# Kernel tuning notes

Hardware: AMD Instinct MI355X
Metric: run time of the kernel (lower is better)

The kernel has to match this reference:

```python
import jax, jax.numpy as jnp
import numpy as np

GROUP = 128  # int4 quant group size and Hadamard block size

# Sylvester Hadamard matrix of size 128, orthonormal (H @ H.T = I)
_h = np.array([[1.0]], dtype=np.float32)
while _h.shape[0] < GROUP:
    _h = np.kron(_h, np.array([[1.0, 1.0], [1.0, -1.0]], dtype=np.float32))
H128 = jnp.asarray(_h / np.sqrt(GROUP))


def hadamard_rotate(x):
    # blockwise Hadamard rotation along the last dim (last dim % 128 == 0)
    *lead, n = x.shape
    xr = x.reshape(*lead, n // GROUP, GROUP) @ H128
    return xr.reshape(*lead, n)


def dequant_int4(wq, scales):
    # wq: [out, in] uint4 values in [0,16); scales: [out, in//GROUP]
    out_dim, in_dim = wq.shape
    w = (wq.astype(jnp.float32) - 8.0).reshape(out_dim, in_dim // GROUP, GROUP)
    w = w * scales[:, :, None]
    return w.reshape(out_dim, in_dim)


def rotate_linear_int4(x, wq, scales):
    # y = hadamard(x) @ dequant(W).T
    return hadamard_rotate(x) @ dequant_int4(wq, scales).T


def setup_inputs() -> dict:
    key = jax.random.key(0)
    ks = jax.random.split(key, 7)
    T, D, I = 4096, 4096, 12288  # tokens, hidden, intermediate
    x = jax.random.normal(ks[0], (T, D), dtype=jnp.float32)
    wq_gate = jax.random.randint(ks[1], (I, D), 0, 16, dtype=jnp.int32)
    s_gate = jax.random.uniform(ks[2], (I, D // GROUP), dtype=jnp.float32) * 0.01
    wq_up = jax.random.randint(ks[3], (I, D), 0, 16, dtype=jnp.int32)
    s_up = jax.random.uniform(ks[4], (I, D // GROUP), dtype=jnp.float32) * 0.01
    wq_down = jax.random.randint(ks[5], (D, I), 0, 16, dtype=jnp.int32)
    s_down = jax.random.uniform(ks[6], (D, I // GROUP), dtype=jnp.float32) * 0.01
    return {"x": x, "wq_gate": wq_gate, "s_gate": s_gate,
            "wq_up": wq_up, "s_up": s_up,
            "wq_down": wq_down, "s_down": s_down}


def reference(x, wq_gate, s_gate, wq_up, s_up, wq_down, s_down):
    gate = rotate_linear_int4(x, wq_gate, s_gate)   # [T, I]
    up = rotate_linear_int4(x, wq_up, s_up)         # [T, I]
    h = jax.nn.silu(gate) * up                       # SiluAndMul on cat([gate, up])
    return rotate_linear_int4(h, wq_down, s_down)    # [T, D]
```

## Files before the change

kernel.cpp:

```cpp
#include <hip/hip_runtime.h>
#include <hip/hip_bf16.h>
#include <cstdint>

#define T_DIM 4096
#define D_DIM 4096
#define I_DIM 12288
#define GRP   128

typedef __attribute__((ext_vector_type(8))) short bf16x8;
typedef __attribute__((ext_vector_type(4))) float f32x4;
typedef __attribute__((ext_vector_type(4))) int   int32x4;

typedef __attribute__((address_space(3))) void lds_void;
typedef const __attribute__((address_space(1))) void gmem_void;

static __device__ __forceinline__ unsigned short f2bf(float f) {
    unsigned int u = __float_as_uint(f);
    u += 0x7FFFu + ((u >> 16) & 1u);
    return (unsigned short)(u >> 16);
}
static __device__ __forceinline__ float bf2f(unsigned short b) {
    return __uint_as_float(((unsigned int)b) << 16);
}

__global__ void had_f32_to_bf16(const float* __restrict__ in, unsigned short* __restrict__ out,
                                int ngroups) {
    int gid = blockIdx.x * (blockDim.x >> 6) + (threadIdx.x >> 6);
    if (gid >= ngroups) return;
    int lane = threadIdx.x & 63;
    const float2 v2 = *reinterpret_cast<const float2*>(in + (size_t)gid * 128 + lane * 2);
    float v0 = v2.x, v1 = v2.y;
    { float t0 = v0 + v1, t1 = v0 - v1; v0 = t0; v1 = t1; }
#pragma unroll
    for (int m = 1; m <= 32; m <<= 1) {
        float b0 = __shfl_xor(v0, m);
        float b1 = __shfl_xor(v1, m);
        if (lane & m) { v0 = b0 - v0; v1 = b1 - v1; }
        else          { v0 = v0 + b0; v1 = v1 + b1; }
    }
    const float s = 0.08838834764831843f;
    unsigned int o = (unsigned int)f2bf(v0 * s) | ((unsigned int)f2bf(v1 * s) << 16);
    *reinterpret_cast<unsigned int*>(out + (size_t)gid * 128 + lane * 2) = o;
}

__global__ void had_bf16_inplace(unsigned short* __restrict__ buf, int ngroups) {
    int gid = blockIdx.x * (blockDim.x >> 6) + (threadIdx.x >> 6);
    if (gid >= ngroups) return;
    int lane = threadIdx.x & 63;
    unsigned int pv = *reinterpret_cast<const unsigned int*>(buf + (size_t)gid * 128 + lane * 2);
    float v0 = __uint_as_float((pv & 0xFFFFu) << 16);
    float v1 = __uint_as_float(pv & 0xFFFF0000u);
    { float t0 = v0 + v1, t1 = v0 - v1; v0 = t0; v1 = t1; }
#pragma unroll
    for (int m = 1; m <= 32; m <<= 1) {
        float b0 = __shfl_xor(v0, m);
        float b1 = __shfl_xor(v1, m);
        if (lane & m) { v0 = b0 - v0; v1 = b1 - v1; }
        else          { v0 = v0 + b0; v1 = v1 + b1; }
    }
    const float s = 0.08838834764831843f;
    unsigned int o = (unsigned int)f2bf(v0 * s) | ((unsigned int)f2bf(v1 * s) << 16);
    *reinterpret_cast<unsigned int*>(buf + (size_t)gid * 128 + lane * 2) = o;
}

__global__ void dequant_w(const int* __restrict__ Wq, const float* __restrict__ S,
                          unsigned short* __restrict__ Wbf, int In, int total8) {
    int t = blockIdx.x * blockDim.x + threadIdx.x;
    if (t >= total8) return;
    size_t base = (size_t)t * 8;
    size_t row = base / (size_t)In;
    int col = (int)(base - row * (size_t)In);
    float sc = S[row * (size_t)(In >> 7) + (col >> 7)];
    const int32x4* p = reinterpret_cast<const int32x4*>(Wq + base);
    int32x4 a = p[0], b = p[1];
    float nsc = -8.0f * sc;
    unsigned int o0 = (unsigned int)f2bf((float)a.x * sc + nsc) |
                      ((unsigned int)f2bf((float)a.y * sc + nsc) << 16);
    unsigned int o1 = (unsigned int)f2bf((float)a.z * sc + nsc) |
                      ((unsigned int)f2bf((float)a.w * sc + nsc) << 16);
    unsigned int o2 = (unsigned int)f2bf((float)b.x * sc + nsc) |
                      ((unsigned int)f2bf((float)b.y * sc + nsc) << 16);
    unsigned int o3 = (unsigned int)f2bf((float)b.z * sc + nsc) |
                      ((unsigned int)f2bf((float)b.w * sc + nsc) << 16);
    *reinterpret_cast<uint4*>(Wbf + base) = make_uint4(o0, o1, o2, o3);
}


#define GBAR()  __builtin_amdgcn_s_barrier()
#define VMW(n)  asm volatile("s_waitcnt vmcnt(" #n ")" ::: "memory")
#define P1()    __builtin_amdgcn_s_setprio(1)
#define P0()    __builtin_amdgcn_s_setprio(0)

#define STG(bb, mat, h, kb)                                                            \
  { _Pragma("unroll")                                                                  \
    for (int i_ = 0; i_ < 2; ++i_) {                                                   \
      const int rl_ = (h) * 128 + i_ * 64 + (tid >> 3);                                \
      const int gs_ = (tid & 7) ^ ((tid >> 3) & 7);                                    \
      const unsigned short* gp_ = ((mat) ? W : A) +                                    \
          (size_t)(((mat) ? n0 : m0) + rl_) * K + (kb) + gs_ * 8;                      \
      unsigned short* lp_ = lds + (bb) * 32768 + (mat) * 16384 +                       \
          ((h) * 128 + i_ * 64 + wid * 8) * 64;                                        \
      __builtin_amdgcn_global_load_lds((gmem_void*)gp_, (lds_void*)lp_, 16, 0, 0);     \
    } }

#define LDAQ(dst, bb, q)                                                               \
  _Pragma("unroll")                                                                    \
  for (int mi_ = 0; mi_ < 2; ++mi_)                                                    \
  _Pragma("unroll")                                                                    \
  for (int ks_ = 0; ks_ < 2; ++ks_) {                                                  \
    int r_ = wr * 128 + (q) * 32 + mi_ * 16 + (lane & 15);                             \
    int c_ = ks_ * 4 + kc;                                                             \
    dst[mi_][ks_] = *reinterpret_cast<const bf16x8*>(                                  \
        lds + (bb) * 32768 + r_ * 64 + ((c_ ^ (r_ & 7)) << 3));                        \
  }

#define LDBQ(bb)                                                                       \
  _Pragma("unroll")                                                                    \
  for (int ni_ = 0; ni_ < 4; ++ni_)                                                    \
  _Pragma("unroll")                                                                    \
  for (int ks_ = 0; ks_ < 2; ++ks_) {                                                  \
    int r_ = wc * 64 + ni_ * 16 + (lane & 15);                                         \
    int c_ = ks_ * 4 + kc;                                                             \
    bk[ni_][ks_] = *reinterpret_cast<const bf16x8*>(                                   \
        lds + (bb) * 32768 + 16384 + r_ * 64 + ((c_ ^ (r_ & 7)) << 3));                \
  }

#define MF16(q, afb)                                                                   \
  _Pragma("unroll")                                                                    \
  for (int ks_ = 0; ks_ < 2; ++ks_)                                                    \
  _Pragma("unroll")                                                                    \
  for (int mi_ = 0; mi_ < 2; ++mi_)                                                    \
  _Pragma("unroll")                                                                    \
  for (int ni_ = 0; ni_ < 4; ++ni_)                                                    \
    acc[(q) * 2 + mi_][ni_] = __builtin_amdgcn_mfma_f32_16x16x32_bf16(                 \
        afb[mi_][ks_], bk[ni_][ks_], acc[(q) * 2 + mi_][ni_], 0, 0, 0);

template<int MODE>
__global__ __launch_bounds__(512, 2)
void gemm256(const unsigned short* __restrict__ A,
             const unsigned short* __restrict__ W,
             void* __restrict__ C, int M, int N, int K)
{
    __shared__ __align__(16) unsigned short lds[65536];

    const int MT = M >> 8;
    const int nwg = gridDim.x;
    const int bid = blockIdx.x;
    const int cpx = nwg >> 3;
    const int wg  = (bid & 7) * cpx + (bid >> 3);
    const int m0 = (wg % MT) << 8;
    const int n0 = (wg / MT) << 8;

    const int tid  = threadIdx.x;
    const int lane = tid & 63;
    const int wid  = tid >> 6;
    const int wr = wid >> 2;
    const int wc = wid & 3;
    const int kc = lane >> 4;

    f32x4 acc[8][4];
#pragma unroll
    for (int i = 0; i < 8; ++i)
#pragma unroll
        for (int j = 0; j < 4; ++j) acc[i][j] = (f32x4)0.0f;

    const int NT = K >> 6;
    const int J  = NT >> 1;

    bf16x8 afA[2][2], afB[2][2], bk[4][2];

    STG(0, 0, 0, 0); STG(0, 0, 1, 0);
    STG(0, 1, 0, 0); STG(0, 1, 1, 0);
    VMW(0);
    GBAR();
    LDAQ(afA, 0, 0);
    STG(1, 1, 0, 64); STG(1, 1, 1, 64);

    for (int j = 0; j < J - 1; ++j) {
        const int ka  = (j << 7);
        const int kb1 = ka + 64;
        const int ka2 = ka + 128;
        const int ka3 = ka + 192;
        LDBQ(0); LDAQ(afB, 0, 1); STG(1, 0, 0, kb1);
        GBAR(); P1(); MF16(0, afA); P0(); GBAR();
        LDAQ(afA, 0, 2); STG(1, 0, 1, kb1);
        GBAR(); P1(); MF16(1, afB); P0(); GBAR();
        LDAQ(afB, 0, 3); STG(0, 1, 0, ka2);
        GBAR(); P1(); MF16(2, afA); P0(); GBAR();
        VMW(2); LDAQ(afA, 1, 0); STG(0, 1, 1, ka2);
        GBAR(); P1(); MF16(3, afB); P0(); GBAR();
        LDBQ(1); LDAQ(afB, 1, 1); STG(0, 0, 0, ka2);
        GBAR(); P1(); MF16(0, afA); P0(); GBAR();
        LDAQ(afA, 1, 2); STG(0, 0, 1, ka2);
        GBAR(); P1(); MF16(1, afB); P0(); GBAR();
        LDAQ(afB, 1, 3); STG(1, 1, 0, ka3);
        GBAR(); P1(); MF16(2, afA); P0(); GBAR();
        VMW(2); LDAQ(afA, 0, 0); STG(1, 1, 1, ka3);
        GBAR(); P1(); MF16(3, afB); P0(); GBAR();
    }

    {
        const int kb1 = ((NT - 1) << 6);
        LDBQ(0); LDAQ(afB, 0, 1); STG(1, 0, 0, kb1);
        GBAR(); P1(); MF16(0, afA); P0(); GBAR();
        LDAQ(afA, 0, 2); STG(1, 0, 1, kb1);
        GBAR(); P1(); MF16(1, afB); P0(); GBAR();
        LDAQ(afB, 0, 3);
        GBAR(); P1(); MF16(2, afA); P0(); GBAR();
        VMW(0); LDAQ(afA, 1, 0);
        GBAR(); P1(); MF16(3, afB); P0(); GBAR();
        LDBQ(1); LDAQ(afB, 1, 1);
        GBAR(); P1(); MF16(0, afA); P0(); GBAR();
        LDAQ(afA, 1, 2);
        GBAR(); P1(); MF16(1, afB); P0(); GBAR();
        LDAQ(afB, 1, 3);
        GBAR(); P1(); MF16(2, afA); P0(); GBAR();
        GBAR(); P1(); MF16(3, afB); P0();
    }

#pragma unroll
    for (int mi = 0; mi < 8; ++mi)
#pragma unroll
        for (int ni = 0; ni < 4; ++ni) {
            const int col = n0 + (wc << 6) + ni * 16 + (lane & 15);
#pragma unroll
            for (int r = 0; r < 4; ++r) {
                const int row = m0 + (wr << 7) + mi * 16 + ((lane >> 4) << 2) + r;
                const size_t idx = (size_t)row * N + col;
                if (MODE == 2) {
                    ((float*)C)[idx] = acc[mi][ni][r];
                } else if (MODE == 0) {
                    ((unsigned short*)C)[idx] = f2bf(acc[mi][ni][r]);
                } else {
                    float g = bf2f(((unsigned short*)C)[idx]);
                    float u = acc[mi][ni][r];
                    float h = (g / (1.0f + __expf(-g))) * u;
                    ((unsigned short*)C)[idx] = f2bf(h);
                }
            }
        }
}

__global__ __launch_bounds__(256, 2)
void gemm_gateup_fb(const unsigned short* __restrict__ Xr,
                    const int* __restrict__ Wg, const float* __restrict__ Sg,
                    const int* __restrict__ Wu, const float* __restrict__ Su,
                    unsigned short* __restrict__ H)
{
    __shared__ __align__(16) unsigned short lA [128 * 64];
    __shared__ __align__(16) unsigned short lBg[128 * 64];
    __shared__ __align__(16) unsigned short lBu[128 * 64];
    const int MT = T_DIM / 128;
    const int bid = blockIdx.x;
    const int m0 = (bid % MT) * 128;
    const int n0 = (bid / MT) * 128;
    const int tid  = threadIdx.x;
    const int lane = tid & 63;
    const int wid  = tid >> 6;
    const int wr = wid >> 1, wc = wid & 1;
    f32x4 accG[4][4], accU[4][4];
#pragma unroll
    for (int i = 0; i < 4; ++i)
#pragma unroll
        for (int j = 0; j < 4; ++j) { accG[i][j] = (f32x4)0.0f; accU[i][j] = (f32x4)0.0f; }
    const int arow = lane >> 3;
    const int acol = (lane & 7) * 8;
    const int SStride = D_DIM / GRP;
    for (int k0 = 0; k0 < D_DIM; k0 += 64) {
        __syncthreads();
#pragma unroll
        for (int it = 0; it < 4; ++it) {
            int chunk = wid * 4 + it;
            const unsigned short* gp = Xr + (size_t)(m0 + chunk * 8 + arow) * D_DIM + k0 + acol;
            __builtin_amdgcn_global_load_lds((gmem_void*)gp, (lds_void*)(lA + chunk * 512), 16, 0, 0);
        }
        const int g = k0 >> 7;
#pragma unroll
        for (int i = 0; i < 8; ++i) {
            int linear = i * 1024 + tid * 4;
            int r = linear >> 6;
            int c = linear & 63;
            const int32x4 wg = *reinterpret_cast<const int32x4*>(Wg + (size_t)(n0 + r) * D_DIM + k0 + c);
            const int32x4 wu = *reinterpret_cast<const int32x4*>(Wu + (size_t)(n0 + r) * D_DIM + k0 + c);
            float scg = Sg[(size_t)(n0 + r) * SStride + g];
            float scu = Su[(size_t)(n0 + r) * SStride + g];
            unsigned int g01 = (unsigned int)f2bf((float)(wg.x - 8) * scg) | ((unsigned int)f2bf((float)(wg.y - 8) * scg) << 16);
            unsigned int g23 = (unsigned int)f2bf((float)(wg.z - 8) * scg) | ((unsigned int)f2bf((float)(wg.w - 8) * scg) << 16);
            unsigned int u01 = (unsigned int)f2bf((float)(wu.x - 8) * scu) | ((unsigned int)f2bf((float)(wu.y - 8) * scu) << 16);
            unsigned int u23 = (unsigned int)f2bf((float)(wu.z - 8) * scu) | ((unsigned int)f2bf((float)(wu.w - 8) * scu) << 16);
            *reinterpret_cast<uint2*>(lBg + r * 64 + c) = make_uint2(g01, g23);
            *reinterpret_cast<uint2*>(lBu + r * 64 + c) = make_uint2(u01, u23);
        }
        __syncthreads();
#pragma unroll
        for (int ks = 0; ks < 2; ++ks) {
            const int koff = ks * 32 + (lane >> 4) * 8;
            bf16x8 af[4], bg[4], bu[4];
#pragma unroll
            for (int mi = 0; mi < 4; ++mi)
                af[mi] = *reinterpret_cast<const bf16x8*>(lA + (wr * 64 + mi * 16 + (lane & 15)) * 64 + koff);
#pragma unroll
            for (int ni = 0; ni < 4; ++ni) {
                bg[ni] = *reinterpret_cast<const bf16x8*>(lBg + (wc * 64 + ni * 16 + (lane & 15)) * 64 + koff);
                bu[ni] = *reinterpret_cast<const bf16x8*>(lBu + (wc * 64 + ni * 16 + (lane & 15)) * 64 + koff);
            }
#pragma unroll
            for (int mi = 0; mi < 4; ++mi)
#pragma unroll
                for (int ni = 0; ni < 4; ++ni) {
                    accG[mi][ni] = __builtin_amdgcn_mfma_f32_16x16x32_bf16(af[mi], bg[ni], accG[mi][ni], 0, 0, 0);
                    accU[mi][ni] = __builtin_amdgcn_mfma_f32_16x16x32_bf16(af[mi], bu[ni], accU[mi][ni], 0, 0, 0);
                }
        }
    }
#pragma unroll
    for (int mi = 0; mi < 4; ++mi)
#pragma unroll
        for (int ni = 0; ni < 4; ++ni) {
            const int col = n0 + wc * 64 + ni * 16 + (lane & 15);
#pragma unroll
            for (int r = 0; r < 4; ++r) {
                const int row = m0 + wr * 64 + mi * 16 + (lane >> 4) * 4 + r;
                float gv = accG[mi][ni][r];
                float uv = accU[mi][ni][r];
                float hv = (gv / (1.0f + __expf(-gv))) * uv;
                H[(size_t)row * I_DIM + col] = f2bf(hv);
            }
        }
}

__global__ __launch_bounds__(256, 2)
void gemm_down_fb(const unsigned short* __restrict__ Hr,
                  const int* __restrict__ Wd, const float* __restrict__ Sd,
                  float* __restrict__ Out)
{
    __shared__ __align__(16) unsigned short lA[128 * 64];
    __shared__ __align__(16) unsigned short lB[128 * 64];
    const int MT = T_DIM / 128;
    const int bid = blockIdx.x;
    const int m0 = (bid % MT) * 128;
    const int n0 = (bid / MT) * 128;
    const int tid  = threadIdx.x;
    const int lane = tid & 63;
    const int wid  = tid >> 6;
    const int wr = wid >> 1, wc = wid & 1;
    f32x4 acc[4][4];
#pragma unroll
    for (int i = 0; i < 4; ++i)
#pragma unroll
        for (int j = 0; j < 4; ++j) acc[i][j] = (f32x4)0.0f;
    const int arow = lane >> 3;
    const int acol = (lane & 7) * 8;
    const int SStride = I_DIM / GRP;
    for (int k0 = 0; k0 < I_DIM; k0 += 64) {
        __syncthreads();
#pragma unroll
        for (int it = 0; it < 4; ++it) {
            int chunk = wid * 4 + it;
            const unsigned short* gp = Hr + (size_t)(m0 + chunk * 8 + arow) * I_DIM + k0 + acol;
            __builtin_amdgcn_global_load_lds((gmem_void*)gp, (lds_void*)(lA + chunk * 512), 16, 0, 0);
        }
        const int g = k0 >> 7;
#pragma unroll
        for (int i = 0; i < 8; ++i) {
            int linear = i * 1024 + tid * 4;
            int r = linear >> 6;
            int c = linear & 63;
            const int32x4 wd = *reinterpret_cast<const int32x4*>(Wd + (size_t)(n0 + r) * I_DIM + k0 + c);
            float sc = Sd[(size_t)(n0 + r) * SStride + g];
            unsigned int d01 = (unsigned int)f2bf((float)(wd.x - 8) * sc) | ((unsigned int)f2bf((float)(wd.y - 8) * sc) << 16);
            unsigned int d23 = (unsigned int)f2bf((float)(wd.z - 8) * sc) | ((unsigned int)f2bf((float)(wd.w - 8) * sc) << 16);
            *reinterpret_cast<uint2*>(lB + r * 64 + c) = make_uint2(d01, d23);
        }
        __syncthreads();
#pragma unroll
        for (int ks = 0; ks < 2; ++ks) {
            const int koff = ks * 32 + (lane >> 4) * 8;
            bf16x8 af[4], bfr[4];
#pragma unroll
            for (int mi = 0; mi < 4; ++mi)
                af[mi] = *reinterpret_cast<const bf16x8*>(lA + (wr * 64 + mi * 16 + (lane & 15)) * 64 + koff);
#pragma unroll
            for (int ni = 0; ni < 4; ++ni)
                bfr[ni] = *reinterpret_cast<const bf16x8*>(lB + (wc * 64 + ni * 16 + (lane & 15)) * 64 + koff);
#pragma unroll
            for (int mi = 0; mi < 4; ++mi)
#pragma unroll
                for (int ni = 0; ni < 4; ++ni)
                    acc[mi][ni] = __builtin_amdgcn_mfma_f32_16x16x32_bf16(af[mi], bfr[ni], acc[mi][ni], 0, 0, 0);
        }
    }
#pragma unroll
    for (int mi = 0; mi < 4; ++mi)
#pragma unroll
        for (int ni = 0; ni < 4; ++ni) {
            const int col = n0 + wc * 64 + ni * 16 + (lane & 15);
#pragma unroll
            for (int r = 0; r < 4; ++r) {
                const int row = m0 + wr * 64 + mi * 16 + (lane >> 4) * 4 + r;
                Out[(size_t)row * D_DIM + col] = acc[mi][ni][r];
            }
        }
}

extern "C" void kernel_launch(void* const* d_in, const int* in_sizes, int n_in,
                              void* d_out, int out_size, void* d_ws, size_t ws_size,
                              hipStream_t stream) {
    const float* x       = (const float*)d_in[0];
    const int*   wq_gate = (const int*)d_in[1];
    const float* s_gate  = (const float*)d_in[2];
    const int*   wq_up   = (const int*)d_in[3];
    const float* s_up    = (const float*)d_in[4];
    const int*   wq_down = (const int*)d_in[5];
    const float* s_down  = (const float*)d_in[6];
    float* out = (float*)d_out;

    const size_t XR_E = (size_t)T_DIM * D_DIM;
    const size_t H_E  = (size_t)T_DIM * I_DIM;
    const size_t W_E  = (size_t)I_DIM * D_DIM;
    const size_t need = (XR_E + H_E + 2 * W_E) * sizeof(unsigned short);

    unsigned short* xr = (unsigned short*)d_ws;
    unsigned short* h  = xr + XR_E;

    {
        int ngroups = (int)(XR_E / 128);
        had_f32_to_bf16<<<dim3(ngroups / 4), dim3(256), 0, stream>>>(x, xr, ngroups);
    }

    if (ws_size >= need) {
        unsigned short* wgbf = h + H_E;
        unsigned short* wubf = wgbf + W_E;
        int total8 = (int)(W_E / 8);
        dequant_w<<<dim3((total8 + 255) / 256), dim3(256), 0, stream>>>(wq_gate, s_gate, wgbf, D_DIM, total8);
        dequant_w<<<dim3((total8 + 255) / 256), dim3(256), 0, stream>>>(wq_up,   s_up,   wubf, D_DIM, total8);
        gemm256<0><<<dim3((T_DIM / 256) * (I_DIM / 256)), dim3(512), 0, stream>>>(
            xr, wgbf, (void*)h, T_DIM, I_DIM, D_DIM);
        gemm256<1><<<dim3((T_DIM / 256) * (I_DIM / 256)), dim3(512), 0, stream>>>(
            xr, wubf, (void*)h, T_DIM, I_DIM, D_DIM);
        {
            int ngroups = (int)(H_E / 128);
            had_bf16_inplace<<<dim3(ngroups / 4), dim3(256), 0, stream>>>(h, ngroups);
        }
        dequant_w<<<dim3((total8 + 255) / 256), dim3(256), 0, stream>>>(wq_down, s_down, wgbf, I_DIM, total8);
        gemm256<2><<<dim3((T_DIM / 256) * (D_DIM / 256)), dim3(512), 0, stream>>>(
            h, wgbf, (void*)out, T_DIM, D_DIM, I_DIM);
    } else {
        gemm_gateup_fb<<<dim3((T_DIM / 128) * (I_DIM / 128)), dim3(256), 0, stream>>>(
            xr, wq_gate, s_gate, wq_up, s_up, h);
        {
            int ngroups = (int)(H_E / 128);
            had_bf16_inplace<<<dim3(ngroups / 4), dim3(256), 0, stream>>>(h, ngroups);
        }
        gemm_down_fb<<<dim3((T_DIM / 128) * (D_DIM / 128)), dim3(256), 0, stream>>>(
            h, wq_down, s_down, out);
    }
}
```

Baseline: 1.278 ms.

## Restructure GEMM main loop into half-tile phases with single A fragment buffer

Replaces the eight quarter-tile phases per iteration (each 16 MFMAs, double-buffered A fragments) with four half-tile phases of 32 MFMAs each, using a single A fragment array and explicit lgkmcnt waits. Global-to-LDS stages are issued in pairs and the vmcnt waits and the prologue ordering are adjusted to match. The goal is fewer barriers and larger MFMA bursts per sync. In exchange, LDS reads no longer overlap the previous phase's MFMAs, so latency may be more exposed.

```diff
diff --git a/kernel.cpp b/kernel.cpp
--- a/kernel.cpp
+++ b/kernel.cpp
@@ -87,6 +87,7 @@
 
 
 #define GBAR()  __builtin_amdgcn_s_barrier()
+#define LGKM0() asm volatile("s_waitcnt lgkmcnt(0)" ::: "memory")
 #define VMW(n)  asm volatile("s_waitcnt vmcnt(" #n ")" ::: "memory")
 #define P1()    __builtin_amdgcn_s_setprio(1)
 #define P0()    __builtin_amdgcn_s_setprio(0)
@@ -103,14 +104,14 @@
       __builtin_amdgcn_global_load_lds((gmem_void*)gp_, (lds_void*)lp_, 16, 0, 0);     \
     } }
 
-#define LDAQ(dst, bb, q)                                                               \
-  _Pragma("unroll")                                                                    \
-  for (int mi_ = 0; mi_ < 2; ++mi_)                                                    \
+#define LDAH(bb, hh)                                                                   \
+  _Pragma("unroll")                                                                    \
+  for (int mi_ = 0; mi_ < 4; ++mi_)                                                    \
   _Pragma("unroll")                                                                    \
   for (int ks_ = 0; ks_ < 2; ++ks_) {                                                  \
-    int r_ = wr * 128 + (q) * 32 + mi_ * 16 + (lane & 15);                             \
+    int r_ = wr * 128 + (hh) * 64 + mi_ * 16 + (lane & 15);                            \
     int c_ = ks_ * 4 + kc;                                                             \
-    dst[mi_][ks_] = *reinterpret_cast<const bf16x8*>(                                  \
+    af[mi_][ks_] = *reinterpret_cast<const bf16x8*>(                                   \
         lds + (bb) * 32768 + r_ * 64 + ((c_ ^ (r_ & 7)) << 3));                        \
   }
 
@@ -125,15 +126,15 @@
         lds + (bb) * 32768 + 16384 + r_ * 64 + ((c_ ^ (r_ & 7)) << 3));                \
   }
 
-#define MF16(q, afb)                                                                   \
+#define MF32(hh)                                                                       \
   _Pragma("unroll")                                                                    \
   for (int ks_ = 0; ks_ < 2; ++ks_)                                                    \
   _Pragma("unroll")                                                                    \
-  for (int mi_ = 0; mi_ < 2; ++mi_)                                                    \
+  for (int mi_ = 0; mi_ < 4; ++mi_)                                                    \
   _Pragma("unroll")                                                                    \
   for (int ni_ = 0; ni_ < 4; ++ni_)                                                    \
-    acc[(q) * 2 + mi_][ni_] = __builtin_amdgcn_mfma_f32_16x16x32_bf16(                 \
-        afb[mi_][ks_], bk[ni_][ks_], acc[(q) * 2 + mi_][ni_], 0, 0, 0);
+    acc[(hh) * 4 + mi_][ni_] = __builtin_amdgcn_mfma_f32_16x16x32_bf16(                \
+        af[mi_][ks_], bk[ni_][ks_], acc[(hh) * 4 + mi_][ni_], 0, 0, 0);
 
 template<int MODE>
 __global__ __launch_bounds__(512, 2)
@@ -167,55 +168,44 @@
     const int NT = K >> 6;
     const int J  = NT >> 1;
 
-    bf16x8 afA[2][2], afB[2][2], bk[4][2];
+    bf16x8 af[4][2], bk[4][2];
 
     STG(0, 0, 0, 0); STG(0, 0, 1, 0);
     STG(0, 1, 0, 0); STG(0, 1, 1, 0);
-    VMW(0);
+    STG(1, 1, 0, 64); STG(1, 1, 1, 64);
+    VMW(4);
     GBAR();
-    LDAQ(afA, 0, 0);
-    STG(1, 1, 0, 64); STG(1, 1, 1, 64);
 
     for (int j = 0; j < J - 1; ++j) {
         const int ka  = (j << 7);
         const int kb1 = ka + 64;
         const int ka2 = ka + 128;
         const int ka3 = ka + 192;
-        LDBQ(0); LDAQ(afB, 0, 1); STG(1, 0, 0, kb1);
-        GBAR(); P1(); MF16(0, afA); P0(); GBAR();
-        LDAQ(afA, 0, 2); STG(1, 0, 1, kb1);
-        GBAR(); P1(); MF16(1, afB); P0(); GBAR();
-        LDAQ(afB, 0, 3); STG(0, 1, 0, ka2);
-        GBAR(); P1(); MF16(2, afA); P0(); GBAR();
-        VMW(2); LDAQ(afA, 1, 0); STG(0, 1, 1, ka2);
-        GBAR(); P1(); MF16(3, afB); P0(); GBAR();
-        LDBQ(1); LDAQ(afB, 1, 1); STG(0, 0, 0, ka2);
-        GBAR(); P1(); MF16(0, afA); P0(); GBAR();
-        LDAQ(afA, 1, 2); STG(0, 0, 1, ka2);
-        GBAR(); P1(); MF16(1, afB); P0(); GBAR();
-        LDAQ(afB, 1, 3); STG(1, 1, 0, ka3);
-        GBAR(); P1(); MF16(2, afA); P0(); GBAR();
-        VMW(2); LDAQ(afA, 0, 0); STG(1, 1, 1, ka3);
-        GBAR(); P1(); MF16(3, afB); P0(); GBAR();
+        LDBQ(0); LDAH(0, 0);
+        STG(1, 0, 0, kb1); STG(1, 0, 1, kb1);
+        GBAR(); LGKM0(); P1(); MF32(0); P0(); GBAR();
+        LDAH(0, 1);
+        STG(0, 1, 0, ka2); STG(0, 1, 1, ka2);
+        GBAR(); LGKM0(); P1(); MF32(1); P0(); VMW(4); GBAR();
+        LDBQ(1); LDAH(1, 0);
+        STG(0, 0, 0, ka2); STG(0, 0, 1, ka2);
+        GBAR(); LGKM0(); P1(); MF32(0); P0(); GBAR();
+        LDAH(1, 1);
+        STG(1, 1, 0, ka3); STG(1, 1, 1, ka3);
+        GBAR(); LGKM0(); P1(); MF32(1); P0(); VMW(4); GBAR();
     }
 
     {
         const int kb1 = ((NT - 1) << 6);
-        LDBQ(0); LDAQ(afB, 0, 1); STG(1, 0, 0, kb1);
-        GBAR(); P1(); MF16(0, afA); P0(); GBAR();
-        LDAQ(afA, 0, 2); STG(1, 0, 1, kb1);
-        GBAR(); P1(); MF16(1, afB); P0(); GBAR();
-        LDAQ(afB, 0, 3);
-        GBAR(); P1(); MF16(2, afA); P0(); GBAR();
-        VMW(0); LDAQ(afA, 1, 0);
-        GBAR(); P1(); MF16(3, afB); P0(); GBAR();
-        LDBQ(1); LDAQ(afB, 1, 1);
-        GBAR(); P1(); MF16(0, afA); P0(); GBAR();
-        LDAQ(afA, 1, 2);
-        GBAR(); P1(); MF16(1, afB); P0(); GBAR();
-        LDAQ(afB, 1, 3);
-        GBAR(); P1(); MF16(2, afA); P0(); GBAR();
-        GBAR(); P1(); MF16(3, afB); P0();
+        LDBQ(0); LDAH(0, 0);
+        STG(1, 0, 0, kb1); STG(1, 0, 1, kb1);
+        GBAR(); LGKM0(); P1(); MF32(0); P0(); GBAR();
+        LDAH(0, 1);
+        GBAR(); LGKM0(); P1(); MF32(1); P0(); VMW(0); GBAR();
+        LDBQ(1); LDAH(1, 0);
+        GBAR(); LGKM0(); P1(); MF32(0); P0(); GBAR();
+        LDAH(1, 1);
+        GBAR(); LGKM0(); P1(); MF32(1); P0();
     }
 
 #pragma unroll
```

After: 1.324 ms. 1.04x slower.
